# Kernel tuning notes

Hardware: AMD Instinct MI355X
Metric: run time of the kernel (lower is better)

The kernel has to match this reference:

```python
import jax, jax.numpy as jnp
import numpy as np

N_NODES = 100000
N_EDGES = 1600000
F_IN = 39
H = 64
N_LAYERS = 2
LN_EPS = 1e-5


def setup_inputs() -> dict:
    key = jax.random.key(0)
    ks = jax.random.split(key, 16)
    s = lambda fan_in: 1.0 / np.sqrt(fan_in)
    inp = {
        "x": jax.random.normal(ks[0], (N_NODES, F_IN), dtype=jnp.float32),
        "edge_index": jax.random.randint(ks[1], (2, N_EDGES), 0, N_NODES, dtype=jnp.int64),
        "W_in": jax.random.uniform(ks[2], (F_IN, H), jnp.float32, -s(F_IN), s(F_IN)),
        "b_in": jnp.zeros((H,), jnp.float32),
        # per-layer stacked params: [n_layers, ...]
        "msg_W": jax.random.uniform(ks[3], (N_LAYERS, 2 * H, H), jnp.float32, -s(2 * H), s(2 * H)),
        "msg_b": jnp.zeros((N_LAYERS, H), jnp.float32),
        "upd_W": jax.random.uniform(ks[4], (N_LAYERS, 2 * H, H), jnp.float32, -s(2 * H), s(2 * H)),
        "upd_b": jnp.zeros((N_LAYERS, H), jnp.float32),
        "ln_g": jnp.ones((N_LAYERS, H), jnp.float32),
        "ln_b": jnp.zeros((N_LAYERS, H), jnp.float32),
        "out_W1": jax.random.uniform(ks[5], (H, H // 2), jnp.float32, -s(H), s(H)),
        "out_b1": jnp.zeros((H // 2,), jnp.float32),
        "out_W2": jax.random.uniform(ks[6], (H // 2, 1), jnp.float32, -s(H // 2), s(H // 2)),
        "out_b2": jnp.zeros((1,), jnp.float32),
    }
    return inp


def _layernorm(z, g, b):
    mu = jnp.mean(z, axis=-1, keepdims=True)
    var = jnp.mean(jnp.square(z - mu), axis=-1, keepdims=True)
    return (z - mu) * jax.lax.rsqrt(var + LN_EPS) * g + b


def reference(x, edge_index, W_in, b_in, msg_W, msg_b, upd_W, upd_b,
              ln_g, ln_b, out_W1, out_b1, out_W2, out_b2):
    n = x.shape[0]
    row, col = edge_index[0], edge_index[1]
    h = x @ W_in + b_in  # [N, H]
    ones = jnp.ones((col.shape[0], 1), h.dtype)
    cnt = jax.ops.segment_sum(ones, col, num_segments=n)  # in-degree, [N,1]
    denom = jnp.maximum(cnt, 1.0)
    for l in range(N_LAYERS):
        # gather endpoint features -> edge message MLP
        msg = jnp.concatenate([h[row], h[col]], axis=-1) @ msg_W[l] + msg_b[l]  # [E, H]
        aggr = jax.ops.segment_sum(msg, col, num_segments=n) / denom  # mean-agg, [N, H]
        upd = jnp.concatenate([h, aggr], axis=-1) @ upd_W[l] + upd_b[l]
        h = _layernorm(h + upd, ln_g[l], ln_b[l])
    o = jax.nn.gelu(h @ out_W1 + out_b1, approximate=False) @ out_W2 + out_b2  # [N, 1]
    return jax.nn.sigmoid(o[..., 0])  # [N]
```

## Files before the change

kernel.cpp:

```cpp
#include <hip/hip_runtime.h>
#include <math.h>
#include <stdint.h>

#define H 64
#define FIN 39
#define PB 512
#define NRSH 9
#define NBUK_MAX 256

typedef _Float16 half8 __attribute__((ext_vector_type(8)));
typedef _Float16 half4 __attribute__((ext_vector_type(4)));
typedef float floatx4 __attribute__((ext_vector_type(4)));

__global__ void k_hist(const int* __restrict__ col, int* __restrict__ hist,
                       int E, int nbuk, int chunk) {
    __shared__ int hc[NBUK_MAX];
    int b = blockIdx.x;
    for (int i = threadIdx.x; i < nbuk; i += 256) hc[i] = 0;
    __syncthreads();
    int lo = b * chunk, hi = min(E, lo + chunk);
    for (int e = lo + threadIdx.x; e < hi; e += 256)
        atomicAdd(&hc[col[e] >> NRSH], 1);
    __syncthreads();
    for (int i = threadIdx.x; i < nbuk; i += 256) hist[i * PB + b] = hc[i];
}

__global__ void k_scanA(const int* __restrict__ in, int* __restrict__ out,
                        int* __restrict__ bsum, int M) {
    __shared__ int lds[256];
    int tid = threadIdx.x;
    int i = blockIdx.x * 256 + tid;
    int v = (i < M) ? in[i] : 0;
    lds[tid] = v;
    __syncthreads();
    int acc = v;
    for (int off = 1; off < 256; off <<= 1) {
        int t = (tid >= off) ? lds[tid - off] : 0;
        __syncthreads();
        acc += t;
        lds[tid] = acc;
        __syncthreads();
    }
    if (i < M) out[i] = acc - v;
    if (tid == 255) bsum[blockIdx.x] = acc;
}

__global__ void k_scan2(int* __restrict__ bsum, int nb) {
    __shared__ int lds[512];
    int tid = threadIdx.x;
    int v = (tid < nb) ? bsum[tid] : 0;
    lds[tid] = v;
    __syncthreads();
    int acc = v;
    for (int off = 1; off < 512; off <<= 1) {
        int t = (tid >= off) ? lds[tid - off] : 0;
        __syncthreads();
        acc += t;
        lds[tid] = acc;
        __syncthreads();
    }
    if (tid < nb) bsum[tid] = acc - v;
}

__global__ void k_scanC(int* __restrict__ out, const int* __restrict__ bsum, int M) {
    int i = blockIdx.x * 256 + threadIdx.x;
    if (i < M) out[i] += bsum[blockIdx.x];
}

__global__ void k_part(const int* __restrict__ row, const int* __restrict__ col,
                       const int* __restrict__ hscan, int2* __restrict__ pairs,
                       int E, int nbuk, int chunk) {
    __shared__ int cur[NBUK_MAX];
    int b = blockIdx.x;
    for (int i = threadIdx.x; i < nbuk; i += 256) cur[i] = hscan[i * PB + b];
    __syncthreads();
    int lo = b * chunk, hi = min(E, lo + chunk);
    for (int e = lo + threadIdx.x; e < hi; e += 256) {
        int c = col[e];
        int r = row[e];
        int pos = atomicAdd(&cur[c >> NRSH], 1);
        pairs[pos] = make_int2(c, r);
    }
}

__global__ __launch_bounds__(256) void k_fillb(const int2* __restrict__ pairs,
        const int* __restrict__ hscan, int* __restrict__ csr,
        int* __restrict__ startv, int* __restrict__ deg, float* __restrict__ cnt,
        int E, int N, int nbuk) {
    __shared__ int dh[512];
    __shared__ int sc[256];
    int b = blockIdx.x;
    int tid = threadIdx.x;
    int nlo = b << NRSH;
    int s0 = hscan[b * PB];
    int e0 = (b == nbuk - 1) ? E : hscan[(b + 1) * PB];
    dh[tid] = 0; dh[tid + 256] = 0;
    __syncthreads();
    for (int i = s0 + tid; i < e0; i += 256)
        atomicAdd(&dh[pairs[i].x - nlo], 1);
    __syncthreads();
    int v0 = dh[2 * tid], v1 = dh[2 * tid + 1];
    int ps = v0 + v1;
    sc[tid] = ps;
    __syncthreads();
    int acc = ps;
    for (int off = 1; off < 256; off <<= 1) {
        int t = (tid >= off) ? sc[tid - off] : 0;
        __syncthreads();
        acc += t;
        sc[tid] = acc;
        __syncthreads();
    }
    int excl = acc - ps;
    int o0 = excl, o1 = excl + v0;
    int n0 = nlo + 2 * tid, n1 = n0 + 1;
    if (n0 < N) { startv[n0] = s0 + o0; deg[n0] = v0; cnt[n0] = (float)v0; }
    if (n1 < N) { startv[n1] = s0 + o1; deg[n1] = v1; cnt[n1] = (float)v1; }
    __syncthreads();
    dh[2 * tid] = o0;
    dh[2 * tid + 1] = o1;
    __syncthreads();
    for (int i = s0 + tid; i < e0; i += 256) {
        int2 p = pairs[i];
        int pos = atomicAdd(&dh[p.x - nlo], 1);
        csr[s0 + pos] = p.y;
    }
}

__global__ void k_comb(const float* __restrict__ msgW, const float* __restrict__ msgb,
                       const float* __restrict__ updW, float* __restrict__ waggr,
                       float* __restrict__ wcomb, float* __restrict__ bcomb) {
    int l = blockIdx.x;
    const float* Wmt = msgW + (size_t)l * 2 * H * H;
    const float* Wmb = Wmt + H * H;
    const float* Wu  = updW + (size_t)l * 2 * H * H + H * H;
    const float* mb  = msgb + (size_t)l * H;
    float* WA = waggr + (size_t)l * H * H;
    float* WC = wcomb + (size_t)l * H * H;
    float* bc = bcomb + (size_t)l * H;
    for (int idx = threadIdx.x; idx < H * H; idx += 256) {
        int i = idx >> 6, j = idx & 63;
        float sa = 0.f, sc = 0.f;
        for (int k = 0; k < H; ++k) {
            float wu = Wu[k * H + j];
            sa += Wmt[i * H + k] * wu;
            sc += Wmb[i * H + k] * wu;
        }
        WA[idx] = sa;
        WC[idx] = sc;
    }
    if (threadIdx.x < H) {
        int j = threadIdx.x;
        float s = 0.f;
        for (int k = 0; k < H; ++k) s += mb[k] * Wu[k * H + j];
        bc[j] = s;
    }
}

__global__ void k_pack6(const float* __restrict__ updW, const float* __restrict__ waggr,
                        const float* __restrict__ wcomb, _Float16* __restrict__ ppk) {
    int mat = blockIdx.x;
    const float* W;
    bool addI = false;
    if (mat < 2)      { W = updW + (size_t)mat * 2 * H * H; addI = true; }
    else if (mat < 4) { W = waggr + (size_t)(mat - 2) * H * H; }
    else              { W = wcomb + (size_t)(mat - 4) * H * H; }
    _Float16* dst = ppk + (size_t)mat * 8 * 64 * 8;
    for (int e = threadIdx.x; e < 8 * 64; e += 256) {
        int fidx = e >> 6;
        int ln = e & 63;
        int s = fidx >> 2, t = fidx & 3;
        int kbase = s * 32 + ((ln >> 4) * 8);
        int c = t * 16 + (ln & 15);
        _Float16* d = dst + (size_t)e * 8;
        #pragma unroll
        for (int i = 0; i < 8; ++i) {
            float v = W[(size_t)(kbase + i) * H + c];
            if (addI && (kbase + i) == c) v += 1.0f;
            d[i] = (_Float16)v;
        }
    }
}

__global__ void k_packO(const float* __restrict__ W1, _Float16* __restrict__ opk) {
    for (int e = threadIdx.x; e < 4 * 64; e += 256) {
        int fidx = e >> 6;
        int ln = e & 63;
        int s = fidx >> 1, t = fidx & 1;
        int kbase = s * 32 + ((ln >> 4) * 8);
        int c = t * 16 + (ln & 15);
        _Float16* d = opk + (size_t)e * 8;
        #pragma unroll
        for (int i = 0; i < 8; ++i)
            d[i] = (_Float16)W1[(size_t)(kbase + i) * 32 + c];
    }
}

__global__ void k_input(const float* __restrict__ x, const float* __restrict__ Win,
                        const float* __restrict__ bin, _Float16* __restrict__ h16, int N) {
    __shared__ float w[FIN * H];
    int tid = threadIdx.x;
    for (int i = tid; i < FIN * H; i += 512) w[i] = Win[i];
    __syncthreads();
    int j = tid & 63;
    int un = __builtin_amdgcn_readfirstlane(blockIdx.x * 32 + (tid >> 6) * 4);
    int n0 = min(un, N - 1), n1 = min(un + 1, N - 1), n2 = min(un + 2, N - 1), n3 = min(un + 3, N - 1);
    const float* x0 = x + (size_t)n0 * FIN;
    const float* x1 = x + (size_t)n1 * FIN;
    const float* x2 = x + (size_t)n2 * FIN;
    const float* x3 = x + (size_t)n3 * FIN;
    float a0 = 0.f, a1 = 0.f, a2 = 0.f, a3 = 0.f;
    #pragma unroll
    for (int k = 0; k < FIN; ++k) {
        float wv = w[k * H + j];
        a0 += x0[k] * wv;
        a1 += x1[k] * wv;
        a2 += x2[k] * wv;
        a3 += x3[k] * wv;
    }
    float bj = bin[j];
    if (un     < N) h16[(size_t)n0 * H + j] = (_Float16)(a0 + bj);
    if (un + 1 < N) h16[(size_t)n1 * H + j] = (_Float16)(a1 + bj);
    if (un + 2 < N) h16[(size_t)n2 * H + j] = (_Float16)(a2 + bj);
    if (un + 3 < N) h16[(size_t)n3 * H + j] = (_Float16)(a3 + bj);
}

__global__ void k_aggr(const int* __restrict__ startv, const int* __restrict__ deg,
                       const int* __restrict__ csr, const _Float16* __restrict__ A,
                       _Float16* __restrict__ z16, int N) {
    int tid = threadIdx.x;
    int n = __builtin_amdgcn_readfirstlane(blockIdx.x * 4 + (tid >> 6));
    if (n >= N) return;
    int l = tid & 63;
    int q = l >> 4;
    int m = l & 15;
    int s = startv[n];
    int d = deg[n];
    float a0 = 0.f, a1 = 0.f, a2 = 0.f, a3 = 0.f;
    int i = 0;
    for (; i + 16 <= d; i += 16) {
        int r0 = csr[s + i + q];
        int r1 = csr[s + i + 4 + q];
        int r2 = csr[s + i + 8 + q];
        int r3 = csr[s + i + 12 + q];
        half4 h0 = *(const half4*)(A + (size_t)r0 * H + m * 4);
        half4 h1 = *(const half4*)(A + (size_t)r1 * H + m * 4);
        half4 h2 = *(const half4*)(A + (size_t)r2 * H + m * 4);
        half4 h3 = *(const half4*)(A + (size_t)r3 * H + m * 4);
        a0 += ((float)h0[0] + (float)h1[0]) + ((float)h2[0] + (float)h3[0]);
        a1 += ((float)h0[1] + (float)h1[1]) + ((float)h2[1] + (float)h3[1]);
        a2 += ((float)h0[2] + (float)h1[2]) + ((float)h2[2] + (float)h3[2]);
        a3 += ((float)h0[3] + (float)h1[3]) + ((float)h2[3] + (float)h3[3]);
    }
    for (; i + 8 <= d; i += 8) {
        int rA = csr[s + i + q];
        int rB = csr[s + i + 4 + q];
        half4 hA = *(const half4*)(A + (size_t)rA * H + m * 4);
        half4 hB = *(const half4*)(A + (size_t)rB * H + m * 4);
        a0 += (float)hA[0] + (float)hB[0];
        a1 += (float)hA[1] + (float)hB[1];
        a2 += (float)hA[2] + (float)hB[2];
        a3 += (float)hA[3] + (float)hB[3];
    }
    for (; i < d; i += 4) {
        int ii = i + q;
        if (ii < d) {
            int r = csr[s + ii];
            half4 hv = *(const half4*)(A + (size_t)r * H + m * 4);
            a0 += (float)hv[0];
            a1 += (float)hv[1];
            a2 += (float)hv[2];
            a3 += (float)hv[3];
        }
    }
    a0 += __shfl_xor(a0, 16); a0 += __shfl_xor(a0, 32);
    a1 += __shfl_xor(a1, 16); a1 += __shfl_xor(a1, 32);
    a2 += __shfl_xor(a2, 16); a2 += __shfl_xor(a2, 32);
    a3 += __shfl_xor(a3, 16); a3 += __shfl_xor(a3, 32);
    if (q == 0) {
        half4 hv;
        hv[0] = (_Float16)a0; hv[1] = (_Float16)a1;
        hv[2] = (_Float16)a2; hv[3] = (_Float16)a3;
        *(half4*)(z16 + (size_t)n * H + m * 4) = hv;
    }
}

template<bool DO_OUT>
__global__ __launch_bounds__(256) void k_upd(const _Float16* __restrict__ h16in,
        const _Float16* __restrict__ z16, const float* __restrict__ cnt,
        const _Float16* __restrict__ apk, const _Float16* __restrict__ gpk,
        const _Float16* __restrict__ cpk, const _Float16* __restrict__ opk,
        const float* __restrict__ bias, const float* __restrict__ bcomb,
        const float* __restrict__ lng, const float* __restrict__ lnb,
        _Float16* __restrict__ h16out,
        const float* __restrict__ b1, const float* __restrict__ W2,
        const float* __restrict__ b2,
        float* __restrict__ out, int N) {
    __shared__ __align__(16) _Float16 hsall[DO_OUT ? 4 * 16 * 72 : 8];
    int l = threadIdx.x & 63;
    int w = threadIdx.x >> 6;
    int n0 = blockIdx.x * 64 + w * 16;
    int mrow = l & 15, kgrp = l >> 4;
    int nA = min(n0 + mrow, N - 1);
    half8 ah0 = *(const half8*)(h16in + (size_t)nA * H + kgrp * 8);
    half8 ah1 = *(const half8*)(h16in + (size_t)nA * H + 32 + kgrp * 8);
    half8 zf0 = *(const half8*)(z16 + (size_t)nA * H + kgrp * 8);
    half8 zf1 = *(const half8*)(z16 + (size_t)nA * H + 32 + kgrp * 8);
    floatx4 acc[4] = {};
    floatx4 accZ[4] = {};
    floatx4 accC[4] = {};
    #pragma unroll
    for (int s = 0; s < 2; ++s) {
        half8 a = s ? ah1 : ah0;
        half8 z = s ? zf1 : zf0;
        #pragma unroll
        for (int t = 0; t < 4; ++t) {
            half8 bt = *(const half8*)(apk + ((size_t)((s * 4 + t) * 64 + l)) * 8);
            half8 bg = *(const half8*)(gpk + ((size_t)((s * 4 + t) * 64 + l)) * 8);
            half8 bc = *(const half8*)(cpk + ((size_t)((s * 4 + t) * 64 + l)) * 8);
            acc[t]  = __builtin_amdgcn_mfma_f32_16x16x32_f16(a, bt, acc[t], 0, 0, 0);
            accZ[t] = __builtin_amdgcn_mfma_f32_16x16x32_f16(z, bg, accZ[t], 0, 0, 0);
            accC[t] = __builtin_amdgcn_mfma_f32_16x16x32_f16(a, bc, accC[t], 0, 0, 0);
        }
    }
    float bl[4], gl[4], bb2[4], bcl[4];
    #pragma unroll
    for (int t = 0; t < 4; ++t) {
        int j = t * 16 + mrow;
        bl[t] = bias[j]; gl[t] = lng[j]; bb2[t] = lnb[j]; bcl[t] = bcomb[j];
    }
    float4 cnt4 = *(const float4*)(cnt + n0 + kgrp * 4);
    float zt[4][4];
    #pragma unroll
    for (int r = 0; r < 4; ++r) {
        float c = (r == 0) ? cnt4.x : (r == 1) ? cnt4.y : (r == 2) ? cnt4.z : cnt4.w;
        float rdn = 1.0f / fmaxf(c, 1.0f);
        float mk = (c > 0.f) ? 1.0f : 0.0f;
        #pragma unroll
        for (int t = 0; t < 4; ++t)
            zt[t][r] = acc[t][r] + rdn * accZ[t][r] + mk * (accC[t][r] + bcl[t]) + bl[t];
    }
    #pragma unroll
    for (int r = 0; r < 4; ++r) {
        float s = zt[0][r] + zt[1][r] + zt[2][r] + zt[3][r];
        s += __shfl_xor(s, 1); s += __shfl_xor(s, 2);
        s += __shfl_xor(s, 4); s += __shfl_xor(s, 8);
        float mu = s * (1.0f / H);
        float v = 0.f;
        #pragma unroll
        for (int t = 0; t < 4; ++t) { float d = zt[t][r] - mu; v += d * d; }
        v += __shfl_xor(v, 1); v += __shfl_xor(v, 2);
        v += __shfl_xor(v, 4); v += __shfl_xor(v, 8);
        float rinv = rsqrtf(v * (1.0f / H) + 1e-5f);
        int m = kgrp * 4 + r;
        int n = n0 + m;
        #pragma unroll
        for (int t = 0; t < 4; ++t) {
            float hval = (zt[t][r] - mu) * rinv * gl[t] + bb2[t];
            if (DO_OUT) hsall[(w * 16 + m) * 72 + t * 16 + mrow] = (_Float16)hval;
            else if (n < N) h16out[(size_t)n * H + t * 16 + mrow] = (_Float16)hval;
        }
    }
    if (DO_OUT) {
        __syncthreads();
        const _Float16* hs = hsall + w * 16 * 72;
        half8 af0 = *(const half8*)(hs + mrow * 72 + kgrp * 8);
        half8 af1 = *(const half8*)(hs + mrow * 72 + 32 + kgrp * 8);
        floatx4 accO[2] = {};
        #pragma unroll
        for (int s = 0; s < 2; ++s) {
            half8 a = s ? af1 : af0;
            #pragma unroll
            for (int t = 0; t < 2; ++t) {
                half8 b = *(const half8*)(opk + ((size_t)((s * 2 + t) * 64 + l)) * 8);
                accO[t] = __builtin_amdgcn_mfma_f32_16x16x32_f16(a, b, accO[t], 0, 0, 0);
            }
        }
        float b1v0 = b1[mrow], b1v1 = b1[16 + mrow];
        float w2v0 = W2[mrow], w2v1 = W2[16 + mrow];
        float b2v = b2[0];
        #pragma unroll
        for (int r = 0; r < 4; ++r) {
            float t0 = accO[0][r] + b1v0;
            float t1 = accO[1][r] + b1v1;
            float g = 0.5f * t0 * (1.0f + erff(t0 * 0.70710678118654752f)) * w2v0
                    + 0.5f * t1 * (1.0f + erff(t1 * 0.70710678118654752f)) * w2v1;
            g += __shfl_xor(g, 1); g += __shfl_xor(g, 2);
            g += __shfl_xor(g, 4); g += __shfl_xor(g, 8);
            int n = n0 + kgrp * 4 + r;
            if (mrow == 0 && n < N) out[n] = 1.0f / (1.0f + expf(-(g + b2v)));
        }
    }
}

extern "C" void kernel_launch(void* const* d_in, const int* in_sizes, int n_in,
                              void* d_out, int out_size, void* d_ws, size_t ws_size,
                              hipStream_t stream) {
    const float* x    = (const float*)d_in[0];
    const int*   ei   = (const int*)d_in[1];
    const float* Win  = (const float*)d_in[2];
    const float* bin  = (const float*)d_in[3];
    const float* msgW = (const float*)d_in[4];
    const float* msgb = (const float*)d_in[5];
    const float* updW = (const float*)d_in[6];
    const float* updb = (const float*)d_in[7];
    const float* lng  = (const float*)d_in[8];
    const float* lnb  = (const float*)d_in[9];
    const float* W1   = (const float*)d_in[10];
    const float* b1   = (const float*)d_in[11];
    const float* W2   = (const float*)d_in[12];
    const float* b2   = (const float*)d_in[13];

    int N = in_sizes[0] / FIN;
    int E = in_sizes[1] / 2;
    const int* row = ei;
    const int* col = ei + E;

    int nbuk = (N + 511) >> NRSH;
    int M = nbuk * PB;
    int chunk = (E + PB - 1) / PB;

    float* wsp   = (float*)d_ws;
    float* cnt   = wsp;
    float* waggr = wsp + N;
    float* wcomb = waggr + 2 * H * H;
    float* bcomb = wcomb + 2 * H * H;
    _Float16* Z16  = (_Float16*)(bcomb + 2 * H);
    _Float16* h16a = Z16 + (size_t)N * H;
    _Float16* h16b = h16a + (size_t)N * H;
    _Float16* ppk  = h16b + (size_t)N * H;
    _Float16* opk  = ppk + 6 * 4096;
    int* deg    = (int*)(opk + 2048);
    int* startv = deg + N;
    int* bsum   = startv + N;
    int* hist   = bsum + 512;
    int* hscan  = hist + M;
    int* csr    = hscan + M;
    uintptr_t pa = (uintptr_t)(csr + E);
    pa = (pa + 7) & ~(uintptr_t)7;
    int2* pairs = (int2*)pa;

    int nb64 = (N + 63) / 64;
    int scanblk = (M + 255) / 256;

    k_comb<<<2, 256, 0, stream>>>(msgW, msgb, updW, waggr, wcomb, bcomb);
    k_pack6<<<6, 256, 0, stream>>>(updW, waggr, wcomb, ppk);
    k_packO<<<1, 256, 0, stream>>>(W1, opk);

    k_hist<<<PB, 256, 0, stream>>>(col, hist, E, nbuk, chunk);
    k_scanA<<<scanblk, 256, 0, stream>>>(hist, hscan, bsum, M);
    k_scan2<<<1, 512, 0, stream>>>(bsum, scanblk);
    k_scanC<<<scanblk, 256, 0, stream>>>(hscan, bsum, M);
    k_part<<<PB, 256, 0, stream>>>(row, col, hscan, pairs, E, nbuk, chunk);
    k_fillb<<<nbuk, 256, 0, stream>>>(pairs, hscan, csr, startv, deg, cnt, E, N, nbuk);

    k_input<<<(N + 31) / 32, 512, 0, stream>>>(x, Win, bin, h16a, N);

    k_aggr<<<(N + 3) / 4, 256, 0, stream>>>(startv, deg, csr, h16a, Z16, N);
    k_upd<false><<<nb64, 256, 0, stream>>>(h16a, Z16, cnt,
                                           ppk + 0 * 4096, ppk + 2 * 4096, ppk + 4 * 4096,
                                           nullptr, updb, bcomb, lng, lnb, h16b,
                                           nullptr, nullptr, nullptr, nullptr, N);

    k_aggr<<<(N + 3) / 4, 256, 0, stream>>>(startv, deg, csr, h16b, Z16, N);
    k_upd<true><<<nb64, 256, 0, stream>>>(h16b, Z16, cnt,
                                          ppk + 1 * 4096, ppk + 3 * 4096, ppk + 5 * 4096,
                                          opk, updb + H, bcomb + H, lng + H, lnb + H,
                                          nullptr, b1, W2, b2, (float*)d_out, N);
}
```

Measured before the change: 217.7 us.

## Fuse weight prep kernels, drop scan fix-up pass, pack CSR pairs into 32 bits

Merges the three weight-preparation kernels into one launch that computes the combined message/update weights inline. The separate scan fix-up kernel is removed: consumers add the block offset themselves when they read the scan. Partition pairs are packed into one 32-bit word (local node index in the high bits, source row below), which halves the scratch traffic between the partition and fill passes. The partition block count is reduced from 512 to 256, so each block handles a larger chunk of edges. The packing assumes row indices fit in 23 bits.

```diff
diff --git a/kernel.cpp b/kernel.cpp
--- a/kernel.cpp
+++ b/kernel.cpp
@@ -4,7 +4,7 @@
 
 #define H 64
 #define FIN 39
-#define PB 512
+#define PB 256
 #define NRSH 9
 #define NBUK_MAX 256
 
@@ -62,42 +62,46 @@
     if (tid < nb) bsum[tid] = acc - v;
 }
 
-__global__ void k_scanC(int* __restrict__ out, const int* __restrict__ bsum, int M) {
-    int i = blockIdx.x * 256 + threadIdx.x;
-    if (i < M) out[i] += bsum[blockIdx.x];
-}
-
 __global__ void k_part(const int* __restrict__ row, const int* __restrict__ col,
-                       const int* __restrict__ hscan, int2* __restrict__ pairs,
-                       int E, int nbuk, int chunk) {
+                       const int* __restrict__ hscan, const int* __restrict__ bsum,
+                       uint32_t* __restrict__ upairs, int E, int nbuk, int chunk) {
     __shared__ int cur[NBUK_MAX];
     int b = blockIdx.x;
-    for (int i = threadIdx.x; i < nbuk; i += 256) cur[i] = hscan[i * PB + b];
+    for (int i = threadIdx.x; i < nbuk; i += 256) {
+        int g = i * PB + b;
+        cur[i] = hscan[g] + bsum[g >> 8];
+    }
     __syncthreads();
     int lo = b * chunk, hi = min(E, lo + chunk);
     for (int e = lo + threadIdx.x; e < hi; e += 256) {
         int c = col[e];
         int r = row[e];
         int pos = atomicAdd(&cur[c >> NRSH], 1);
-        pairs[pos] = make_int2(c, r);
-    }
-}
-
-__global__ __launch_bounds__(256) void k_fillb(const int2* __restrict__ pairs,
-        const int* __restrict__ hscan, int* __restrict__ csr,
-        int* __restrict__ startv, int* __restrict__ deg, float* __restrict__ cnt,
-        int E, int N, int nbuk) {
+        upairs[pos] = ((uint32_t)(c & 511) << 23) | (uint32_t)r;
+    }
+}
+
+__global__ __launch_bounds__(256) void k_fillb(const uint32_t* __restrict__ upairs,
+        const int* __restrict__ hscan, const int* __restrict__ bsum,
+        int* __restrict__ csr, int* __restrict__ startv, int* __restrict__ deg,
+        float* __restrict__ cnt, int E, int N, int nbuk) {
     __shared__ int dh[512];
     __shared__ int sc[256];
     int b = blockIdx.x;
     int tid = threadIdx.x;
     int nlo = b << NRSH;
-    int s0 = hscan[b * PB];
-    int e0 = (b == nbuk - 1) ? E : hscan[(b + 1) * PB];
+    int g0 = b * PB;
+    int s0 = hscan[g0] + bsum[g0 >> 8];
+    int e0;
+    if (b == nbuk - 1) e0 = E;
+    else {
+        int g1 = (b + 1) * PB;
+        e0 = hscan[g1] + bsum[g1 >> 8];
+    }
     dh[tid] = 0; dh[tid + 256] = 0;
     __syncthreads();
     for (int i = s0 + tid; i < e0; i += 256)
-        atomicAdd(&dh[pairs[i].x - nlo], 1);
+        atomicAdd(&dh[upairs[i] >> 23], 1);
     __syncthreads();
     int v0 = dh[2 * tid], v1 = dh[2 * tid + 1];
     int ps = v0 + v1;
@@ -121,78 +125,69 @@
     dh[2 * tid + 1] = o1;
     __syncthreads();
     for (int i = s0 + tid; i < e0; i += 256) {
-        int2 p = pairs[i];
-        int pos = atomicAdd(&dh[p.x - nlo], 1);
-        csr[s0 + pos] = p.y;
-    }
-}
-
-__global__ void k_comb(const float* __restrict__ msgW, const float* __restrict__ msgb,
-                       const float* __restrict__ updW, float* __restrict__ waggr,
-                       float* __restrict__ wcomb, float* __restrict__ bcomb) {
-    int l = blockIdx.x;
-    const float* Wmt = msgW + (size_t)l * 2 * H * H;
-    const float* Wmb = Wmt + H * H;
-    const float* Wu  = updW + (size_t)l * 2 * H * H + H * H;
-    const float* mb  = msgb + (size_t)l * H;
-    float* WA = waggr + (size_t)l * H * H;
-    float* WC = wcomb + (size_t)l * H * H;
-    float* bc = bcomb + (size_t)l * H;
-    for (int idx = threadIdx.x; idx < H * H; idx += 256) {
-        int i = idx >> 6, j = idx & 63;
-        float sa = 0.f, sc = 0.f;
-        for (int k = 0; k < H; ++k) {
-            float wu = Wu[k * H + j];
-            sa += Wmt[i * H + k] * wu;
-            sc += Wmb[i * H + k] * wu;
-        }
-        WA[idx] = sa;
-        WC[idx] = sc;
-    }
-    if (threadIdx.x < H) {
-        int j = threadIdx.x;
-        float s = 0.f;
-        for (int k = 0; k < H; ++k) s += mb[k] * Wu[k * H + j];
-        bc[j] = s;
-    }
-}
-
-__global__ void k_pack6(const float* __restrict__ updW, const float* __restrict__ waggr,
-                        const float* __restrict__ wcomb, _Float16* __restrict__ ppk) {
+        uint32_t p = upairs[i];
+        int pos = atomicAdd(&dh[p >> 23], 1);
+        csr[s0 + pos] = (int)(p & 0x7FFFFF);
+    }
+}
+
+__global__ void k_prep(const float* __restrict__ msgW, const float* __restrict__ msgb,
+                       const float* __restrict__ updW, const float* __restrict__ W1,
+                       _Float16* __restrict__ ppk, _Float16* __restrict__ opk,
+                       float* __restrict__ bcomb) {
     int mat = blockIdx.x;
-    const float* W;
-    bool addI = false;
-    if (mat < 2)      { W = updW + (size_t)mat * 2 * H * H; addI = true; }
-    else if (mat < 4) { W = waggr + (size_t)(mat - 2) * H * H; }
-    else              { W = wcomb + (size_t)(mat - 4) * H * H; }
-    _Float16* dst = ppk + (size_t)mat * 8 * 64 * 8;
-    for (int e = threadIdx.x; e < 8 * 64; e += 256) {
-        int fidx = e >> 6;
-        int ln = e & 63;
-        int s = fidx >> 2, t = fidx & 3;
-        int kbase = s * 32 + ((ln >> 4) * 8);
-        int c = t * 16 + (ln & 15);
-        _Float16* d = dst + (size_t)e * 8;
-        #pragma unroll
-        for (int i = 0; i < 8; ++i) {
-            float v = W[(size_t)(kbase + i) * H + c];
-            if (addI && (kbase + i) == c) v += 1.0f;
-            d[i] = (_Float16)v;
-        }
-    }
-}
-
-__global__ void k_packO(const float* __restrict__ W1, _Float16* __restrict__ opk) {
-    for (int e = threadIdx.x; e < 4 * 64; e += 256) {
-        int fidx = e >> 6;
-        int ln = e & 63;
-        int s = fidx >> 1, t = fidx & 1;
-        int kbase = s * 32 + ((ln >> 4) * 8);
-        int c = t * 16 + (ln & 15);
-        _Float16* d = opk + (size_t)e * 8;
-        #pragma unroll
-        for (int i = 0; i < 8; ++i)
-            d[i] = (_Float16)W1[(size_t)(kbase + i) * 32 + c];
+    if (mat < 6) {
+        int l = mat & 1;
+        _Float16* dst = ppk + (size_t)mat * 8 * 64 * 8;
+        const float* Wu = updW + (size_t)l * 2 * H * H + H * H;
+        for (int e = threadIdx.x; e < 8 * 64; e += 256) {
+            int fidx = e >> 6;
+            int ln = e & 63;
+            int s = fidx >> 2, t = fidx & 3;
+            int kbase = s * 32 + ((ln >> 4) * 8);
+            int c = t * 16 + (ln & 15);
+            _Float16* d = dst + (size_t)e * 8;
+            if (mat < 2) {
+                const float* W = updW + (size_t)l * 2 * H * H;
+                #pragma unroll
+                for (int i = 0; i < 8; ++i) {
+                    float v = W[(size_t)(kbase + i) * H + c];
+                    if ((kbase + i) == c) v += 1.0f;
+                    d[i] = (_Float16)v;
+                }
+            } else {
+                const float* Wm = (mat < 4) ? (msgW + (size_t)l * 2 * H * H)
+                                            : (msgW + (size_t)l * 2 * H * H + H * H);
+                #pragma unroll
+                for (int i = 0; i < 8; ++i) {
+                    const float* wr = Wm + (size_t)(kbase + i) * H;
+                    float s2 = 0.f;
+                    for (int k = 0; k < H; ++k) s2 += wr[k] * Wu[k * H + c];
+                    d[i] = (_Float16)s2;
+                }
+            }
+        }
+    } else {
+        for (int e = threadIdx.x; e < 4 * 64; e += 256) {
+            int fidx = e >> 6;
+            int ln = e & 63;
+            int s = fidx >> 1, t = fidx & 1;
+            int kbase = s * 32 + ((ln >> 4) * 8);
+            int c = t * 16 + (ln & 15);
+            _Float16* d = opk + (size_t)e * 8;
+            #pragma unroll
+            for (int i = 0; i < 8; ++i)
+                d[i] = (_Float16)W1[(size_t)(kbase + i) * 32 + c];
+        }
+        if (threadIdx.x < 128) {
+            int l = threadIdx.x >> 6;
+            int j = threadIdx.x & 63;
+            const float* Wu = updW + (size_t)l * 2 * H * H + H * H;
+            const float* mb = msgb + (size_t)l * H;
+            float s = 0.f;
+            for (int k = 0; k < H; ++k) s += mb[k] * Wu[k * H + j];
+            bcomb[(size_t)l * H + j] = s;
+        }
     }
 }
 
@@ -422,9 +417,7 @@
 
     float* wsp   = (float*)d_ws;
     float* cnt   = wsp;
-    float* waggr = wsp + N;
-    float* wcomb = waggr + 2 * H * H;
-    float* bcomb = wcomb + 2 * H * H;
+    float* bcomb = wsp + N;
     _Float16* Z16  = (_Float16*)(bcomb + 2 * H);
     _Float16* h16a = Z16 + (size_t)N * H;
     _Float16* h16b = h16a + (size_t)N * H;
@@ -436,23 +429,19 @@
     int* hist   = bsum + 512;
     int* hscan  = hist + M;
     int* csr    = hscan + M;
-    uintptr_t pa = (uintptr_t)(csr + E);
-    pa = (pa + 7) & ~(uintptr_t)7;
-    int2* pairs = (int2*)pa;
+    uint32_t* upairs = (uint32_t*)(csr + E);
 
     int nb64 = (N + 63) / 64;
     int scanblk = (M + 255) / 256;
 
-    k_comb<<<2, 256, 0, stream>>>(msgW, msgb, updW, waggr, wcomb, bcomb);
-    k_pack6<<<6, 256, 0, stream>>>(updW, waggr, wcomb, ppk);
-    k_packO<<<1, 256, 0, stream>>>(W1, opk);
+    k_prep<<<7, 256, 0, stream>>>(msgW, msgb, updW, W1, ppk, opk, bcomb);
 
     k_hist<<<PB, 256, 0, stream>>>(col, hist, E, nbuk, chunk);
     k_scanA<<<scanblk, 256, 0, stream>>>(hist, hscan, bsum, M);
     k_scan2<<<1, 512, 0, stream>>>(bsum, scanblk);
-    k_scanC<<<scanblk, 256, 0, stream>>>(hscan, bsum, M);
-    k_part<<<PB, 256, 0, stream>>>(row, col, hscan, pairs, E, nbuk, chunk);
-    k_fillb<<<nbuk, 256, 0, stream>>>(pairs, hscan, csr, startv, deg, cnt, E, N, nbuk);
+    k_part<<<PB, 256, 0, stream>>>(row, col, hscan, bsum, upairs, E, nbuk, chunk);
+    k_fillb<<<nbuk, 256, 0, stream>>>(upairs, hscan, bsum, csr, startv, deg, cnt,
+                                      E, N, nbuk);
 
     k_input<<<(N + 31) / 32, 512, 0, stream>>>(x, Win, bin, h16a, N);
 
```

Result: faster. 204.8 us (-5.9%).
